# Kernel tuning notes

Measured on AMD Instinct MI355X. Metric: run time of the kernel, lower is better.

The kernel has to match this reference:

```python
import jax, jax.numpy as jnp
import numpy as np

B, N, T, D, O = 8, 1024, 12, 64, 64

def setup_inputs() -> dict:
    key = jax.random.key(0)
    k1, k2, k3 = jax.random.split(key, 3)
    x = jax.random.normal(k1, (B, N, T, D), dtype=jnp.float32)
    # row-normalized random adjacency (dense mask, as in the torch module)
    adj = jax.random.uniform(k2, (N, N), dtype=jnp.float32)
    norm_adj = adj / jnp.sum(adj, axis=-1, keepdims=True)
    theta_w = jax.random.normal(k3, (D, O), dtype=jnp.float32) / np.sqrt(D)
    return {"x": x, "norm_adj": norm_adj, "theta_w": theta_w}

def reference(x, norm_adj, theta_w):
    b, n, t, d = x.shape
    # [B, N, T, D] -> [B*T, N, D]
    xr = jnp.transpose(x, (0, 2, 1, 3)).reshape(b * t, n, d)
    # spatial attention scores [B*T, N, N]
    scores = jnp.einsum('gnd,gmd->gnm', xr, xr) / jnp.sqrt(jnp.float32(d))
    attn = jax.nn.softmax(scores, axis=-1)
    # adjacency-masked attention, then aggregate and project
    agg = jnp.einsum('gnm,gmd->gnd', norm_adj[None, :, :] * attn, xr)
    out = jnp.einsum('gnd,do->gno', agg, theta_w)
    # [B*T, N, O] -> [B, N, T, O], relu
    out = jnp.transpose(out.reshape(b, t, n, -1), (0, 2, 1, 3))
    return jax.nn.relu(out)
```

## Files before the change

### kernel.cpp

```cpp
#include <hip/hip_runtime.h>


#define NB    8
#define NT    12
#define NNODE 1024
#define ND    64
#define XROW  768

typedef __bf16 bf16x8  __attribute__((ext_vector_type(8)));
typedef __bf16 bf16x2  __attribute__((ext_vector_type(2)));
typedef float  floatx4 __attribute__((ext_vector_type(4)));
typedef float  floatx16 __attribute__((ext_vector_type(16)));
typedef unsigned uintx4 __attribute__((ext_vector_type(4)));

#define MFMA32(a,b,c) __builtin_amdgcn_mfma_f32_32x32x16_bf16((a),(b),(c),0,0,0)
#define QSCALE 0.18033688011112042f

#define KSTRIDE 72
#define VSTRIDE 40
#define OFF_KHI 0
#define OFF_KLO 4608
#define OFF_VHI 9216
#define OFF_VLO 14336
#define SMEM_BYTES 19456

struct bfpair { __bf16 h, l; };

__device__ __forceinline__ bfpair split1(float f) {
    bfpair r;
    __bf16 hb = (__bf16)f;
    float hf = __builtin_bit_cast(float,
                   (unsigned)__builtin_bit_cast(unsigned short, hb) << 16);
    r.h = hb;
    r.l = (__bf16)(f - hf);
    return r;
}

__device__ __forceinline__ unsigned pk2(__bf16 a, __bf16 b) {
    bf16x2 t; t[0] = a; t[1] = b;
    return __builtin_bit_cast(unsigned, t);
}

__device__ __forceinline__ bf16x8 xchg(unsigned A0, unsigned A1,
                                       unsigned B0, unsigned B1, int L5) {
    unsigned sA = L5 ? A0 : B0;
    unsigned sB = L5 ? A1 : B1;
    unsigned rA = (unsigned)__shfl_xor((int)sA, 32);
    unsigned rB = (unsigned)__shfl_xor((int)sB, 32);
    uintx4 u;
    u[0] = L5 ? rA : A0;
    u[1] = L5 ? rB : A1;
    u[2] = L5 ? B0 : rA;
    u[3] = L5 ? B1 : rB;
    return __builtin_bit_cast(bf16x8, u);
}

__global__ void __launch_bounds__(256, 2)
spattn(const float* __restrict__ x, const float* __restrict__ adj,
       const float* __restrict__ theta, float* __restrict__ out)
{
    __shared__ __align__(16) char smem[SMEM_BYTES];
    __bf16* Khi = (__bf16*)(smem + OFF_KHI);
    __bf16* Klo = (__bf16*)(smem + OFF_KLO);
    __bf16* Vhi = (__bf16*)(smem + OFF_VHI);
    __bf16* Vlo = (__bf16*)(smem + OFF_VLO);

    const int tid  = threadIdx.x;
    const int wave = tid >> 6;
    const int lane = tid & 63;
    const int q31  = lane & 31;
    const int L5   = lane >> 5;

    const int bx   = blockIdx.x;
    const int g    = bx >> 3;
    const int rblk = bx & 7;
    const int bb   = g / NT;
    const int tt   = g - bb * NT;
    const int row0 = rblk * 128;
    const int wq   = wave * 32;
    const int qglob = row0 + wq + q31;

    const float* xbase = x + (size_t)bb * (NNODE * XROW) + tt * ND;

    bf16x8 qh[4], ql[4];
    {
        const float* qsrc = xbase + (size_t)qglob * XROW;
        #pragma unroll
        for (int dc = 0; dc < 4; ++dc) {
            floatx4 f0 = *(const floatx4*)(qsrc + dc*16 + L5*8);
            floatx4 f1 = *(const floatx4*)(qsrc + dc*16 + L5*8 + 4);
            #pragma unroll
            for (int i = 0; i < 4; ++i) {
                bfpair p0 = split1(f0[i]*QSCALE);
                qh[dc][i]   = p0.h; ql[dc][i]   = p0.l;
                bfpair p1 = split1(f1[i]*QSCALE);
                qh[dc][4+i] = p1.h; ql[dc][4+i] = p1.l;
            }
        }
    }

    floatx16 O0 = {}, O1 = {};
    float lpart = 0.f;

    const int skey = tid >> 3;
    const int sd0  = (tid & 7) * 8;
    const int svd  = tid >> 2;
    const int svk0 = (tid & 3) * 8;
    floatx4 kf0, kf1;
    float vf[8];

    {
        const float* ksrc = xbase + (size_t)skey * XROW + sd0;
        kf0 = *(const floatx4*)ksrc;
        kf1 = *(const floatx4*)(ksrc + 4);
        const float* vsrc = xbase + (size_t)svk0 * XROW + svd;
        #pragma unroll
        for (int i = 0; i < 8; ++i) vf[i] = vsrc[i * XROW];
    }

    for (int ct = 0; ct < 32; ++ct) {
        const int key0 = ct * 32;
        __syncthreads();
        {
            bf16x8 h, l;
            #pragma unroll
            for (int i = 0; i < 4; ++i) {
                bfpair p0 = split1(kf0[i]); h[i]   = p0.h; l[i]   = p0.l;
                bfpair p1 = split1(kf1[i]); h[4+i] = p1.h; l[4+i] = p1.l;
            }
            *(bf16x8*)(Khi + skey*KSTRIDE + sd0) = h;
            *(bf16x8*)(Klo + skey*KSTRIDE + sd0) = l;
            bf16x8 vh, vl;
            #pragma unroll
            for (int i = 0; i < 8; ++i) {
                bfpair p = split1(vf[i]); vh[i] = p.h; vl[i] = p.l;
            }
            *(bf16x8*)(Vhi + svd*VSTRIDE + svk0) = vh;
            *(bf16x8*)(Vlo + svd*VSTRIDE + svk0) = vl;
        }
        __syncthreads();
        if (ct < 31) {
            const int nk = key0 + 32;
            const float* ksrc = xbase + (size_t)(nk + skey) * XROW + sd0;
            kf0 = *(const floatx4*)ksrc;
            kf1 = *(const floatx4*)(ksrc + 4);
            const float* vsrc = xbase + (size_t)(nk + svk0) * XROW + svd;
            #pragma unroll
            for (int i = 0; i < 8; ++i) vf[i] = vsrc[i * XROW];
        }
        floatx4 adjv[4];
        #pragma unroll
        for (int rg = 0; rg < 4; ++rg)
            adjv[rg] = *(const floatx4*)(adj + (size_t)qglob * NNODE
                                         + key0 + rg*8 + L5*4);

        floatx16 ST = {};
        #pragma unroll
        for (int dc = 0; dc < 4; ++dc) {
            bf16x8 kh = *(const bf16x8*)(Khi + q31*KSTRIDE + dc*16 + L5*8);
            bf16x8 kl = *(const bf16x8*)(Klo + q31*KSTRIDE + dc*16 + L5*8);
            ST = MFMA32(kh, qh[dc], ST);
            ST = MFMA32(kl, qh[dc], ST);
            ST = MFMA32(kh, ql[dc], ST);
        }
        __bf16 pth[16], ptl[16];
        #pragma unroll
        for (int r = 0; r < 16; ++r) {
            float w = __builtin_amdgcn_exp2f(ST[r]);
            lpart += w;
            bfpair p = split1(adjv[r >> 2][r & 3] * w);
            pth[r] = p.h; ptl[r] = p.l;
        }
        unsigned GH[4][2], GL[4][2];
        #pragma unroll
        for (int gg = 0; gg < 4; ++gg) {
            GH[gg][0] = pk2(pth[4*gg],   pth[4*gg+1]);
            GH[gg][1] = pk2(pth[4*gg+2], pth[4*gg+3]);
            GL[gg][0] = pk2(ptl[4*gg],   ptl[4*gg+1]);
            GL[gg][1] = pk2(ptl[4*gg+2], ptl[4*gg+3]);
        }
        #pragma unroll
        for (int kc = 0; kc < 2; ++kc) {
            bf16x8 bh = xchg(GH[2*kc][0], GH[2*kc][1],
                             GH[2*kc+1][0], GH[2*kc+1][1], L5);
            bf16x8 bl = xchg(GL[2*kc][0], GL[2*kc][1],
                             GL[2*kc+1][0], GL[2*kc+1][1], L5);
            {
                bf16x8 vh = *(const bf16x8*)(Vhi + q31*VSTRIDE + kc*16 + L5*8);
                bf16x8 vl = *(const bf16x8*)(Vlo + q31*VSTRIDE + kc*16 + L5*8);
                O0 = MFMA32(vh, bh, O0);
                O0 = MFMA32(vl, bh, O0);
                O0 = MFMA32(vh, bl, O0);
            }
            {
                bf16x8 vh = *(const bf16x8*)(Vhi + (32+q31)*VSTRIDE + kc*16 + L5*8);
                bf16x8 vl = *(const bf16x8*)(Vlo + (32+q31)*VSTRIDE + kc*16 + L5*8);
                O1 = MFMA32(vh, bh, O1);
                O1 = MFMA32(vl, bh, O1);
                O1 = MFMA32(vh, bl, O1);
            }
        }
    }

    float l = lpart + __shfl_xor(lpart, 32);
    float linv = 1.0f / l;

    bf16x8 th[2][4], tlo[2][4];
    #pragma unroll
    for (int ot = 0; ot < 2; ++ot)
        #pragma unroll
        for (int kc = 0; kc < 4; ++kc)
            #pragma unroll
            for (int j = 0; j < 8; ++j) {
                float tv = theta[(size_t)(kc*16 + L5*8 + j) * ND + ot*32 + q31];
                bfpair p = split1(tv);
                th[ot][kc][j] = p.h; tlo[ot][kc][j] = p.l;
            }

    __bf16 agh[32], agl[32];
    #pragma unroll
    for (int r = 0; r < 16; ++r) {
        bfpair p = split1(O0[r] * linv);
        agh[r] = p.h; agl[r] = p.l;
    }
    #pragma unroll
    for (int r = 0; r < 16; ++r) {
        bfpair p = split1(O1[r] * linv);
        agh[16+r] = p.h; agl[16+r] = p.l;
    }
    unsigned AH[8][2], AL[8][2];
    #pragma unroll
    for (int gg = 0; gg < 8; ++gg) {
        AH[gg][0] = pk2(agh[4*gg],   agh[4*gg+1]);
        AH[gg][1] = pk2(agh[4*gg+2], agh[4*gg+3]);
        AL[gg][0] = pk2(agl[4*gg],   agl[4*gg+1]);
        AL[gg][1] = pk2(agl[4*gg+2], agl[4*gg+3]);
    }

    floatx16 OC0 = {}, OC1 = {};
    #pragma unroll
    for (int kc = 0; kc < 4; ++kc) {
        bf16x8 bh = xchg(AH[2*kc][0], AH[2*kc][1],
                         AH[2*kc+1][0], AH[2*kc+1][1], L5);
        bf16x8 bl = xchg(AL[2*kc][0], AL[2*kc][1],
                         AL[2*kc+1][0], AL[2*kc+1][1], L5);
        OC0 = MFMA32(th[0][kc], bh, OC0);
        OC0 = MFMA32(tlo[0][kc], bh, OC0);
        OC0 = MFMA32(th[0][kc], bl, OC0);
        OC1 = MFMA32(th[1][kc], bh, OC1);
        OC1 = MFMA32(tlo[1][kc], bh, OC1);
        OC1 = MFMA32(th[1][kc], bl, OC1);
    }

    float* obase = out + (size_t)bb * (NNODE * XROW) + tt * ND
                       + (size_t)qglob * XROW;
    #pragma unroll
    for (int rg = 0; rg < 4; ++rg) {
        floatx4 v0, v1;
        #pragma unroll
        for (int i = 0; i < 4; ++i) {
            float a = OC0[4*rg + i]; v0[i] = a > 0.f ? a : 0.f;
            float b = OC1[4*rg + i]; v1[i] = b > 0.f ? b : 0.f;
        }
        *(floatx4*)(obase + 8*rg + 4*L5)      = v0;
        *(floatx4*)(obase + 32 + 8*rg + 4*L5) = v1;
    }
}

extern "C" void kernel_launch(void* const* d_in, const int* in_sizes, int n_in,
                              void* d_out, int out_size, void* d_ws, size_t ws_size,
                              hipStream_t stream) {
    (void)in_sizes; (void)n_in; (void)d_ws; (void)ws_size; (void)out_size;
    const float* x     = (const float*)d_in[0];
    const float* adj   = (const float*)d_in[1];
    const float* theta = (const float*)d_in[2];
    float* out = (float*)d_out;
    spattn<<<dim3(768), dim3(256), 0, stream>>>(x, adj, theta, out);
}
```

Measured before the change: 176.2 us.

## Double-buffer K/V tiles in LDS and split MFMA accumulator chains

Moves the K/V tiles in shared memory to a two-buffer ping-pong. The next tile is converted and stored while the current one is consumed, which cuts two barriers per iteration to one and prefetches global loads two tiles ahead. It also splits the score and output MFMA accumulations into independent chains to break dependent MFMA latency. Block-to-work mapping changes so that consecutive blocks handle different (b,t) groups rather than row blocks of the same group. LDS use doubles and accumulator registers grow, which may affect occupancy at launch bounds of 2 blocks.

Result: slower. 180.0 us (+2.1%).

```diff
diff --git a/kernel.cpp b/kernel.cpp
--- a/kernel.cpp
+++ b/kernel.cpp
@@ -22,7 +22,8 @@
 #define OFF_KLO 4608
 #define OFF_VHI 9216
 #define OFF_VLO 14336
-#define SMEM_BYTES 19456
+#define BUFBYTES 19456
+#define SMEM_BYTES (2*BUFBYTES)
 
 struct bfpair { __bf16 h, l; };
 
@@ -60,10 +61,6 @@
        const float* __restrict__ theta, float* __restrict__ out)
 {
     __shared__ __align__(16) char smem[SMEM_BYTES];
-    __bf16* Khi = (__bf16*)(smem + OFF_KHI);
-    __bf16* Klo = (__bf16*)(smem + OFF_KLO);
-    __bf16* Vhi = (__bf16*)(smem + OFF_VHI);
-    __bf16* Vlo = (__bf16*)(smem + OFF_VLO);
 
     const int tid  = threadIdx.x;
     const int wave = tid >> 6;
@@ -72,13 +69,12 @@
     const int L5   = lane >> 5;
 
     const int bx   = blockIdx.x;
-    const int g    = bx >> 3;
-    const int rblk = bx & 7;
+    const int g    = bx % 96;
+    const int rblk = bx / 96;
     const int bb   = g / NT;
     const int tt   = g - bb * NT;
     const int row0 = rblk * 128;
-    const int wq   = wave * 32;
-    const int qglob = row0 + wq + q31;
+    const int qglob = row0 + wave*32 + q31;
 
     const float* xbase = x + (size_t)bb * (NNODE * XROW) + tt * ND;
 
@@ -99,8 +95,8 @@
         }
     }
 
-    floatx16 O0 = {}, O1 = {};
-    float lpart = 0.f;
+    floatx16 O0a = {}, O0b = {}, O1a = {}, O1b = {};
+    float lpA = 0.f, lpB = 0.f;
 
     const int skey = tid >> 3;
     const int sd0  = (tid & 7) * 8;
@@ -116,31 +112,62 @@
         const float* vsrc = xbase + (size_t)svk0 * XROW + svd;
         #pragma unroll
         for (int i = 0; i < 8; ++i) vf[i] = vsrc[i * XROW];
-    }
+
+        bf16x8 h, l;
+        #pragma unroll
+        for (int i = 0; i < 4; ++i) {
+            bfpair p0 = split1(kf0[i]); h[i]   = p0.h; l[i]   = p0.l;
+            bfpair p1 = split1(kf1[i]); h[4+i] = p1.h; l[4+i] = p1.l;
+        }
+        *(bf16x8*)(smem + OFF_KHI + skey*144 + sd0*2) = h;
+        *(bf16x8*)(smem + OFF_KLO + skey*144 + sd0*2) = l;
+        bf16x8 vh, vl;
+        #pragma unroll
+        for (int i = 0; i < 8; ++i) {
+            bfpair p = split1(vf[i]); vh[i] = p.h; vl[i] = p.l;
+        }
+        *(bf16x8*)(smem + OFF_VHI + svd*80 + svk0*2) = vh;
+        *(bf16x8*)(smem + OFF_VLO + svd*80 + svk0*2) = vl;
+
+        const float* ksrc1 = xbase + (size_t)(32 + skey) * XROW + sd0;
+        kf0 = *(const floatx4*)ksrc1;
+        kf1 = *(const floatx4*)(ksrc1 + 4);
+        const float* vsrc1 = xbase + (size_t)(32 + svk0) * XROW + svd;
+        #pragma unroll
+        for (int i = 0; i < 8; ++i) vf[i] = vsrc1[i * XROW];
+    }
+    __syncthreads();
 
     for (int ct = 0; ct < 32; ++ct) {
         const int key0 = ct * 32;
-        __syncthreads();
-        {
+        const char* cur = smem + (ct & 1) * BUFBYTES;
+        char* nxt = smem + ((ct + 1) & 1) * BUFBYTES;
+
+        floatx4 adjv[4];
+        #pragma unroll
+        for (int rg = 0; rg < 4; ++rg)
+            adjv[rg] = *(const floatx4*)(adj + (size_t)qglob * NNODE
+                                         + key0 + rg*8 + L5*4);
+
+        if (ct < 31) {
             bf16x8 h, l;
             #pragma unroll
             for (int i = 0; i < 4; ++i) {
                 bfpair p0 = split1(kf0[i]); h[i]   = p0.h; l[i]   = p0.l;
                 bfpair p1 = split1(kf1[i]); h[4+i] = p1.h; l[4+i] = p1.l;
             }
-            *(bf16x8*)(Khi + skey*KSTRIDE + sd0) = h;
-            *(bf16x8*)(Klo + skey*KSTRIDE + sd0) = l;
+            *(bf16x8*)(nxt + OFF_KHI + skey*144 + sd0*2) = h;
+            *(bf16x8*)(nxt + OFF_KLO + skey*144 + sd0*2) = l;
             bf16x8 vh, vl;
             #pragma unroll
             for (int i = 0; i < 8; ++i) {
                 bfpair p = split1(vf[i]); vh[i] = p.h; vl[i] = p.l;
             }
-            *(bf16x8*)(Vhi + svd*VSTRIDE + svk0) = vh;
-            *(bf16x8*)(Vlo + svd*VSTRIDE + svk0) = vl;
-        }
-        __syncthreads();
-        if (ct < 31) {
-            const int nk = key0 + 32;
+            *(bf16x8*)(nxt + OFF_VHI + svd*80 + svk0*2) = vh;
+            *(bf16x8*)(nxt + OFF_VLO + svd*80 + svk0*2) = vl;
+        }
+        if (ct < 30) {
+            const int nk = key0 + 64;
             const float* ksrc = xbase + (size_t)(nk + skey) * XROW + sd0;
             kf0 = *(const floatx4*)ksrc;
             kf1 = *(const floatx4*)(ksrc + 4);
@@ -148,26 +175,22 @@
             #pragma unroll
             for (int i = 0; i < 8; ++i) vf[i] = vsrc[i * XROW];
         }
-        floatx4 adjv[4];
-        #pragma unroll
-        for (int rg = 0; rg < 4; ++rg)
-            adjv[rg] = *(const floatx4*)(adj + (size_t)qglob * NNODE
-                                         + key0 + rg*8 + L5*4);
-
-        floatx16 ST = {};
+
+        floatx16 STa = {}, STb = {}, STc = {};
         #pragma unroll
         for (int dc = 0; dc < 4; ++dc) {
-            bf16x8 kh = *(const bf16x8*)(Khi + q31*KSTRIDE + dc*16 + L5*8);
-            bf16x8 kl = *(const bf16x8*)(Klo + q31*KSTRIDE + dc*16 + L5*8);
-            ST = MFMA32(kh, qh[dc], ST);
-            ST = MFMA32(kl, qh[dc], ST);
-            ST = MFMA32(kh, ql[dc], ST);
+            bf16x8 kh = *(const bf16x8*)(cur + OFF_KHI + q31*144 + (dc*16 + L5*8)*2);
+            bf16x8 kl = *(const bf16x8*)(cur + OFF_KLO + q31*144 + (dc*16 + L5*8)*2);
+            STa = MFMA32(kh, qh[dc], STa);
+            STb = MFMA32(kl, qh[dc], STb);
+            STc = MFMA32(kh, ql[dc], STc);
         }
         __bf16 pth[16], ptl[16];
         #pragma unroll
         for (int r = 0; r < 16; ++r) {
-            float w = __builtin_amdgcn_exp2f(ST[r]);
-            lpart += w;
+            float s = (STa[r] + STb[r]) + STc[r];
+            float w = __builtin_amdgcn_exp2f(s);
+            if (r & 1) lpB += w; else lpA += w;
             bfpair p = split1(adjv[r >> 2][r & 3] * w);
             pth[r] = p.h; ptl[r] = p.l;
         }
@@ -185,23 +208,21 @@
                              GH[2*kc+1][0], GH[2*kc+1][1], L5);
             bf16x8 bl = xchg(GL[2*kc][0], GL[2*kc][1],
                              GL[2*kc+1][0], GL[2*kc+1][1], L5);
-            {
-                bf16x8 vh = *(const bf16x8*)(Vhi + q31*VSTRIDE + kc*16 + L5*8);
-                bf16x8 vl = *(const bf16x8*)(Vlo + q31*VSTRIDE + kc*16 + L5*8);
-                O0 = MFMA32(vh, bh, O0);
-                O0 = MFMA32(vl, bh, O0);
-                O0 = MFMA32(vh, bl, O0);
-            }
-            {
-                bf16x8 vh = *(const bf16x8*)(Vhi + (32+q31)*VSTRIDE + kc*16 + L5*8);
-                bf16x8 vl = *(const bf16x8*)(Vlo + (32+q31)*VSTRIDE + kc*16 + L5*8);
-                O1 = MFMA32(vh, bh, O1);
-                O1 = MFMA32(vl, bh, O1);
-                O1 = MFMA32(vh, bl, O1);
-            }
-        }
-    }
-
+            bf16x8 v0h = *(const bf16x8*)(cur + OFF_VHI + q31*80      + (kc*16 + L5*8)*2);
+            bf16x8 v0l = *(const bf16x8*)(cur + OFF_VLO + q31*80      + (kc*16 + L5*8)*2);
+            bf16x8 v1h = *(const bf16x8*)(cur + OFF_VHI + (32+q31)*80 + (kc*16 + L5*8)*2);
+            bf16x8 v1l = *(const bf16x8*)(cur + OFF_VLO + (32+q31)*80 + (kc*16 + L5*8)*2);
+            O0a = MFMA32(v0h, bh, O0a);
+            O1a = MFMA32(v1h, bh, O1a);
+            O0b = MFMA32(v0l, bh, O0b);
+            O1b = MFMA32(v1l, bh, O1b);
+            O0b = MFMA32(v0h, bl, O0b);
+            O1b = MFMA32(v1h, bl, O1b);
+        }
+        __syncthreads();
+    }
+
+    float lpart = lpA + lpB;
     float l = lpart + __shfl_xor(lpart, 32);
     float linv = 1.0f / l;
 
@@ -220,12 +241,12 @@
     __bf16 agh[32], agl[32];
     #pragma unroll
     for (int r = 0; r < 16; ++r) {
-        bfpair p = split1(O0[r] * linv);
+        bfpair p = split1((O0a[r] + O0b[r]) * linv);
         agh[r] = p.h; agl[r] = p.l;
     }
     #pragma unroll
     for (int r = 0; r < 16; ++r) {
-        bfpair p = split1(O1[r] * linv);
+        bfpair p = split1((O1a[r] + O1b[r]) * linv);
         agh[16+r] = p.h; agl[16+r] = p.l;
     }
     unsigned AH[8][2], AL[8][2];
@@ -245,10 +266,10 @@
         bf16x8 bl = xchg(AL[2*kc][0], AL[2*kc][1],
                          AL[2*kc+1][0], AL[2*kc+1][1], L5);
         OC0 = MFMA32(th[0][kc], bh, OC0);
+        OC1 = MFMA32(th[1][kc], bh, OC1);
         OC0 = MFMA32(tlo[0][kc], bh, OC0);
+        OC1 = MFMA32(tlo[1][kc], bh, OC1);
         OC0 = MFMA32(th[0][kc], bl, OC0);
-        OC1 = MFMA32(th[1][kc], bh, OC1);
-        OC1 = MFMA32(tlo[1][kc], bh, OC1);
         OC1 = MFMA32(th[1][kc], bl, OC1);
     }
 
```

## Split key range across two wave groups per block and merge partials in LDS

Applied to the files above, without the earlier changes.

Doubles the block to 512 threads, with two groups of four waves each processing half of the 1024 keys for the same 128 query rows, each group using its own shared-memory buffer. Afterward the second group writes its partial O accumulators and row sums to LDS, and the first group adds them before the projection and store. The block index mapping changes so consecutive blocks cover different (batch, time) slices. The final MFMAs are also interleaved across the two accumulators. This is meant to raise occupancy and latency hiding and halve the serial key loop, at the cost of an extra reduction through LDS and more shared memory per block.

Result: slower. 542.3 us (+207.8%).

```diff
diff --git a/kernel.cpp b/kernel.cpp
--- a/kernel.cpp
+++ b/kernel.cpp
@@ -22,7 +22,8 @@
 #define OFF_KLO 4608
 #define OFF_VHI 9216
 #define OFF_VLO 14336
-#define SMEM_BYTES 19456
+#define BUFBYTES 19456
+#define SMEM_BYTES (2*BUFBYTES)
 
 struct bfpair { __bf16 h, l; };
 
@@ -55,32 +56,31 @@
     return __builtin_bit_cast(bf16x8, u);
 }
 
-__global__ void __launch_bounds__(256, 2)
+__global__ void __launch_bounds__(512, 6)
 spattn(const float* __restrict__ x, const float* __restrict__ adj,
        const float* __restrict__ theta, float* __restrict__ out)
 {
     __shared__ __align__(16) char smem[SMEM_BYTES];
-    __bf16* Khi = (__bf16*)(smem + OFF_KHI);
-    __bf16* Klo = (__bf16*)(smem + OFF_KLO);
-    __bf16* Vhi = (__bf16*)(smem + OFF_VHI);
-    __bf16* Vlo = (__bf16*)(smem + OFF_VLO);
 
     const int tid  = threadIdx.x;
     const int wave = tid >> 6;
+    const int grp  = wave >> 2;
+    const int w4   = wave & 3;
     const int lane = tid & 63;
     const int q31  = lane & 31;
     const int L5   = lane >> 5;
 
     const int bx   = blockIdx.x;
-    const int g    = bx >> 3;
-    const int rblk = bx & 7;
+    const int g    = bx % 96;
+    const int rblk = bx / 96;
     const int bb   = g / NT;
     const int tt   = g - bb * NT;
     const int row0 = rblk * 128;
-    const int wq   = wave * 32;
-    const int qglob = row0 + wq + q31;
+    const int qglob = row0 + w4*32 + q31;
+    const int keybase = grp * 512;
 
     const float* xbase = x + (size_t)bb * (NNODE * XROW) + tt * ND;
+    char* buf = smem + grp * BUFBYTES;
 
     bf16x8 qh[4], ql[4];
     {
@@ -102,24 +102,25 @@
     floatx16 O0 = {}, O1 = {};
     float lpart = 0.f;
 
-    const int skey = tid >> 3;
-    const int sd0  = (tid & 7) * 8;
-    const int svd  = tid >> 2;
-    const int svk0 = (tid & 3) * 8;
+    const int t8   = tid & 255;
+    const int skey = t8 >> 3;
+    const int sd0  = (t8 & 7) * 8;
+    const int svd  = t8 >> 2;
+    const int svk0 = (t8 & 3) * 8;
     floatx4 kf0, kf1;
     float vf[8];
 
     {
-        const float* ksrc = xbase + (size_t)skey * XROW + sd0;
+        const float* ksrc = xbase + (size_t)(keybase + skey) * XROW + sd0;
         kf0 = *(const floatx4*)ksrc;
         kf1 = *(const floatx4*)(ksrc + 4);
-        const float* vsrc = xbase + (size_t)svk0 * XROW + svd;
+        const float* vsrc = xbase + (size_t)(keybase + svk0) * XROW + svd;
         #pragma unroll
         for (int i = 0; i < 8; ++i) vf[i] = vsrc[i * XROW];
     }
 
-    for (int ct = 0; ct < 32; ++ct) {
-        const int key0 = ct * 32;
+    for (int ct = 0; ct < 16; ++ct) {
+        const int key0 = keybase + ct * 32;
         __syncthreads();
         {
             bf16x8 h, l;
@@ -128,18 +129,18 @@
                 bfpair p0 = split1(kf0[i]); h[i]   = p0.h; l[i]   = p0.l;
                 bfpair p1 = split1(kf1[i]); h[4+i] = p1.h; l[4+i] = p1.l;
             }
-            *(bf16x8*)(Khi + skey*KSTRIDE + sd0) = h;
-            *(bf16x8*)(Klo + skey*KSTRIDE + sd0) = l;
+            *(bf16x8*)(buf + OFF_KHI + skey*144 + sd0*2) = h;
+            *(bf16x8*)(buf + OFF_KLO + skey*144 + sd0*2) = l;
             bf16x8 vh, vl;
             #pragma unroll
             for (int i = 0; i < 8; ++i) {
                 bfpair p = split1(vf[i]); vh[i] = p.h; vl[i] = p.l;
             }
-            *(bf16x8*)(Vhi + svd*VSTRIDE + svk0) = vh;
-            *(bf16x8*)(Vlo + svd*VSTRIDE + svk0) = vl;
+            *(bf16x8*)(buf + OFF_VHI + svd*80 + svk0*2) = vh;
+            *(bf16x8*)(buf + OFF_VLO + svd*80 + svk0*2) = vl;
         }
         __syncthreads();
-        if (ct < 31) {
+        if (ct < 15) {
             const int nk = key0 + 32;
             const float* ksrc = xbase + (size_t)(nk + skey) * XROW + sd0;
             kf0 = *(const floatx4*)ksrc;
@@ -157,8 +158,8 @@
         floatx16 ST = {};
         #pragma unroll
         for (int dc = 0; dc < 4; ++dc) {
-            bf16x8 kh = *(const bf16x8*)(Khi + q31*KSTRIDE + dc*16 + L5*8);
-            bf16x8 kl = *(const bf16x8*)(Klo + q31*KSTRIDE + dc*16 + L5*8);
+            bf16x8 kh = *(const bf16x8*)(buf + OFF_KHI + q31*144 + (dc*16 + L5*8)*2);
+            bf16x8 kl = *(const bf16x8*)(buf + OFF_KLO + q31*144 + (dc*16 + L5*8)*2);
             ST = MFMA32(kh, qh[dc], ST);
             ST = MFMA32(kl, qh[dc], ST);
             ST = MFMA32(kh, ql[dc], ST);
@@ -186,15 +187,15 @@
             bf16x8 bl = xchg(GL[2*kc][0], GL[2*kc][1],
                              GL[2*kc+1][0], GL[2*kc+1][1], L5);
             {
-                bf16x8 vh = *(const bf16x8*)(Vhi + q31*VSTRIDE + kc*16 + L5*8);
-                bf16x8 vl = *(const bf16x8*)(Vlo + q31*VSTRIDE + kc*16 + L5*8);
+                bf16x8 vh = *(const bf16x8*)(buf + OFF_VHI + q31*80 + (kc*16 + L5*8)*2);
+                bf16x8 vl = *(const bf16x8*)(buf + OFF_VLO + q31*80 + (kc*16 + L5*8)*2);
                 O0 = MFMA32(vh, bh, O0);
                 O0 = MFMA32(vl, bh, O0);
                 O0 = MFMA32(vh, bl, O0);
             }
             {
-                bf16x8 vh = *(const bf16x8*)(Vhi + (32+q31)*VSTRIDE + kc*16 + L5*8);
-                bf16x8 vl = *(const bf16x8*)(Vlo + (32+q31)*VSTRIDE + kc*16 + L5*8);
+                bf16x8 vh = *(const bf16x8*)(buf + OFF_VHI + (32+q31)*80 + (kc*16 + L5*8)*2);
+                bf16x8 vl = *(const bf16x8*)(buf + OFF_VLO + (32+q31)*80 + (kc*16 + L5*8)*2);
                 O1 = MFMA32(vh, bh, O1);
                 O1 = MFMA32(vl, bh, O1);
                 O1 = MFMA32(vh, bl, O1);
@@ -202,6 +203,27 @@
         }
     }
 
+    float* CB = (float*)smem;
+    __syncthreads();
+    if (grp == 1) {
+        const int base = w4*64 + lane;
+        #pragma unroll
+        for (int r = 0; r < 16; ++r) CB[r*256 + base] = O0[r];
+        #pragma unroll
+        for (int r = 0; r < 16; ++r) CB[(16+r)*256 + base] = O1[r];
+        CB[32*256 + base] = lpart;
+    }
+    __syncthreads();
+    if (grp == 1) return;
+
+    {
+        const int base = w4*64 + lane;
+        #pragma unroll
+        for (int r = 0; r < 16; ++r) O0[r] += CB[r*256 + base];
+        #pragma unroll
+        for (int r = 0; r < 16; ++r) O1[r] += CB[(16+r)*256 + base];
+        lpart += CB[32*256 + base];
+    }
     float l = lpart + __shfl_xor(lpart, 32);
     float linv = 1.0f / l;
 
@@ -245,10 +267,10 @@
         bf16x8 bl = xchg(AL[2*kc][0], AL[2*kc][1],
                          AL[2*kc+1][0], AL[2*kc+1][1], L5);
         OC0 = MFMA32(th[0][kc], bh, OC0);
+        OC1 = MFMA32(th[1][kc], bh, OC1);
         OC0 = MFMA32(tlo[0][kc], bh, OC0);
+        OC1 = MFMA32(tlo[1][kc], bh, OC1);
         OC0 = MFMA32(th[0][kc], bl, OC0);
-        OC1 = MFMA32(th[1][kc], bh, OC1);
-        OC1 = MFMA32(tlo[1][kc], bh, OC1);
         OC1 = MFMA32(th[1][kc], bl, OC1);
     }
 
@@ -275,5 +297,5 @@
     const float* adj   = (const float*)d_in[1];
     const float* theta = (const float*)d_in[2];
     float* out = (float*)d_out;
-    spattn<<<dim3(768), dim3(256), 0, stream>>>(x, adj, theta, out);
-}
+    spattn<<<dim3(768), dim3(512), 0, stream>>>(x, adj, theta, out);
+}
```
